# Kernel optimization log

Measured on AMD Instinct MI355X. Metric: run time of the kernel, lower is better.

## Reference

```python
import jax, jax.numpy as jnp
import numpy as np

# SLAYER neuron / simulation constants (from netParams yaml)
THETA = 10.0      # spike threshold
TAU_SR = 10.0     # PSP (SRM) time constant, ms
TS = 1.0          # simulation time step, ms
TAU_RHO = 1.0     # surrogate-gradient width
SCALE_RHO = 1.0   # surrogate-gradient scale
N_TIME_BINS = 300 # tSample / Ts


@jax.custom_vjp
def spike_fn(u):
    # Hard threshold forward; surrogate gradient backward (SLAYER escape-rate pdf).
    return (u >= THETA).astype(u.dtype)

def _spike_fwd(u):
    return spike_fn(u), u

def _spike_bwd(u, g):
    return (g * SCALE_RHO * jnp.exp(-jnp.abs(u - THETA) / TAU_RHO),)

spike_fn.defvjp(_spike_fwd, _spike_bwd)


def psp(x):
    # Causal leaky-integrator (first-order SRM) filter over time.
    # x: [B, T, F] -> u[t] = decay * u[t-1] + x[t]
    decay = jnp.exp(jnp.asarray(-TS / TAU_SR, x.dtype))
    xT = jnp.swapaxes(x, 0, 1)  # [T, B, F]
    def step(u, xt):
        u = decay * u + xt
        return u, u
    _, out = jax.lax.scan(step, jnp.zeros_like(xT[0]), xT)
    return jnp.swapaxes(out, 0, 1)  # [B, T, F]


def rate_encode(inp, n_time_bins, key):
    # Bernoulli rate coding: spike prob per time bin = pixel intensity in [0,1].
    # inp: [B, C, H, W] -> spikes: [B, T, C*H*W]
    B = inp.shape[0]
    probs = inp.reshape(B, 1, -1)  # [B, 1, F]
    u = jax.random.uniform(key, (B, n_time_bins, probs.shape[-1]), dtype=inp.dtype)
    return (u < probs).astype(inp.dtype)


def setup_inputs() -> dict:
    key = jax.random.key(0)
    k1, k2, k3 = jax.random.split(key, 3)
    B, C, H, W = 32, 3, 32, 32
    F_in, F_hid, F_out = C * H * W, 410, 10
    inp = jax.random.uniform(k1, (B, C, H, W), dtype=jnp.float32)
    W1 = jax.random.normal(k2, (F_hid, F_in), dtype=jnp.float32) / np.sqrt(F_in).astype(np.float32)
    W2 = jax.random.normal(k3, (F_out, F_hid), dtype=jnp.float32) / np.sqrt(F_hid).astype(np.float32)
    return {"inp": inp, "W1": W1, "W2": W2}


def reference(inp, W1, W2):
    spikes = rate_encode(inp, N_TIME_BINS, jax.random.key(42))   # [B, T, 3072]
    a1 = jnp.einsum('btf,of->bto', spikes, W1)                    # dense per time bin
    s1 = spike_fn(psp(a1))                                        # [B, T, 410]
    a2 = jnp.einsum('btf,of->bto', s1, W2)
    s2 = spike_fn(psp(a2))                                        # [B, T, 10]
    return jnp.swapaxes(s2, 1, 2)                                 # [B, 10, T]
```

## Files before the change

kernel.cpp:

```cpp
#include <hip/hip_runtime.h>
#include <stdint.h>

#define B_SZ 32
#define T_SZ 300
#define F_IN 3072
#define F_HID 410
#define F_OUT 10
#define M_SZ (B_SZ * T_SZ)
#define N_PAD 448
#define KW (F_IN / 32)
#define TOTAL_ELEMS (B_SZ * T_SZ * F_IN)
#define N_WORDS (TOTAL_ELEMS / 32)
#define A2_STRIDE 16
#define NCHUNK 10
#define CLEN 30
#define NKB (F_IN / 256)
#define MT_CNT (M_SZ / 64)
#define W1_BLOCKS 672
#define RNG_BLOCKS 14400

#define DECAY 0.90483741803595957f
#define THETA 10.0f
#define KS2 (0x1BD11BDAu ^ 42u)

typedef __attribute__((ext_vector_type(8))) int i32x8;
typedef __attribute__((ext_vector_type(16))) float f32x16;

#define TF_R(r) { x0 += x1; \
  asm("v_alignbit_b32 %0, %1, %1, %2" : "=v"(x1) : "v"(x1), "n"(32 - (r))); \
  x1 ^= x0; }

__device__ __forceinline__ uint32_t tf_bits(uint32_t x1i) {
  uint32_t x0 = 0u, x1 = x1i;
  TF_R(13) TF_R(15) TF_R(26) TF_R(6)
  x0 += 42u; x1 += KS2 + 1u;
  TF_R(17) TF_R(29) TF_R(16) TF_R(24)
  x0 += KS2; x1 += 2u;
  TF_R(13) TF_R(15) TF_R(26) TF_R(6)
  x1 += 42u + 3u;
  TF_R(17) TF_R(29) TF_R(16) TF_R(24)
  x0 += 42u; x1 += KS2 + 4u;
  TF_R(13) TF_R(15) TF_R(26) TF_R(6)
  x0 += KS2; x1 += 5u;
  return x0 ^ x1;
}

__device__ __forceinline__ void gld16(const void* g, void* l) {
  __builtin_amdgcn_global_load_lds(
      (const __attribute__((address_space(1))) uint32_t*)g,
      (__attribute__((address_space(3))) uint32_t*)l, 16, 0, 0);
}

__global__ __launch_bounds__(256) void prep(const float* __restrict__ inp,
                                            const float* __restrict__ W1,
                                            uint8_t* __restrict__ W1s,
                                            uint32_t* __restrict__ sbitsT) {
  if (blockIdx.x < W1_BLOCKS) {
    int idx = blockIdx.x * 256 + threadIdx.x;
    int g = idx * 8;
    int n = g / F_IN;
    int k = g - n * F_IN;
    uint32_t d0 = 0u, d1 = 0u;
    if (n < F_HID) {
      const float* s = W1 + (size_t)n * F_IN + k;
      float4 v0 = ((const float4*)s)[0];
      float4 v1 = ((const float4*)s)[1];
      int t0 = __builtin_amdgcn_cvt_pk_fp8_f32(v0.x, v0.y, 0, false);
      t0 = __builtin_amdgcn_cvt_pk_fp8_f32(v0.z, v0.w, t0, true);
      int t1 = __builtin_amdgcn_cvt_pk_fp8_f32(v1.x, v1.y, 0, false);
      t1 = __builtin_amdgcn_cvt_pk_fp8_f32(v1.z, v1.w, t1, true);
      d0 = (uint32_t)t0; d1 = (uint32_t)t1;
    }
    int nt = n >> 6, r = n & 63;
    int kb = k >> 8, c = (k >> 4) & 15, half = (k >> 3) & 1;
    size_t dst = ((((size_t)nt * NKB + kb) * 64 + r) * 16 + (c ^ (r & 15))) * 16 + half * 8;
    *(uint2*)(W1s + dst) = make_uint2(d0, d1);
  } else {
    uint32_t idx = (blockIdx.x - W1_BLOCKS) * 256u + threadIdx.x;
    uint32_t q = idx & 3u;
    uint32_t j = idx >> 2;
    uint32_t r = j & 63u;
    uint32_t t1 = j >> 6;
    uint32_t wi = t1 & 7u;
    uint32_t t2 = t1 >> 3;
    uint32_t kb = t2 % (uint32_t)NKB;
    uint32_t mt = t2 / (uint32_t)NKB;
    uint32_t m = mt * 64u + r;
    uint32_t b = m / (uint32_t)T_SZ;
    uint32_t f = (kb * 8u + wi) * 32u + q * 8u;
    const float* p = inp + b * F_IN + f;
    float4 va = ((const float4*)p)[0];
    float4 vb = ((const float4*)p)[1];
    uint32_t T0 = (uint32_t)ceilf(va.x * 8388608.0f);
    uint32_t T1 = (uint32_t)ceilf(va.y * 8388608.0f);
    uint32_t T2 = (uint32_t)ceilf(va.z * 8388608.0f);
    uint32_t T3 = (uint32_t)ceilf(va.w * 8388608.0f);
    uint32_t T4 = (uint32_t)ceilf(vb.x * 8388608.0f);
    uint32_t T5 = (uint32_t)ceilf(vb.y * 8388608.0f);
    uint32_t T6 = (uint32_t)ceilf(vb.z * 8388608.0f);
    uint32_t T7 = (uint32_t)ceilf(vb.w * 8388608.0f);
    uint32_t b42 = m * (uint32_t)F_IN + f + 42u;
    uint32_t w = 0u;
#define GEN(jj, Tn) { uint32_t bits = tf_bits(b42 + (jj)); \
  w |= ((bits >> 9) < (Tn)) ? (1u << (jj)) : 0u; }
    GEN(0, T0) GEN(1, T1) GEN(2, T2) GEN(3, T3)
    GEN(4, T4) GEN(5, T5) GEN(6, T6) GEN(7, T7)
#undef GEN
    ((uint8_t*)sbitsT)[idx] = (uint8_t)w;
  }
}

__global__ __launch_bounds__(256) void gemm1(const uint32_t* __restrict__ sbitsT,
                                             const uint8_t* __restrict__ W1s,
                                             float* __restrict__ a1) {
  __shared__ uint32_t sAT[8 * 64];
  __shared__ uint8_t sB[64 * 256];

  const int tid = threadIdx.x;
  const int mtile = blockIdx.x;
  const int nt = blockIdx.y;
  const int m0 = mtile * 64;
  const int n0 = nt * 64;
  const int wv = tid >> 6, lane = tid & 63;
  const int wm = (wv & 1) * 32, wn = (wv >> 1) * 32;
  const int l31 = lane & 31, lh = lane >> 5;

  const uint8_t* gB0 = W1s + (size_t)nt * NKB * 16384;
  const uint8_t* gA0 = (const uint8_t*)sbitsT + (size_t)mtile * NKB * 2048;

  f32x16 acc;
#pragma unroll
  for (int e = 0; e < 16; ++e) acc[e] = 0.0f;

  for (int kb = 0; kb < NKB; ++kb) {
    const uint8_t* gB = gB0 + (size_t)kb * 16384;
#pragma unroll
    for (int q = 0; q < 4; ++q)
      gld16(gB + (wv * 4 + q) * 1024 + lane * 16, &sB[(wv * 4 + q) * 1024]);
    if (wv < 2)
      gld16(gA0 + (size_t)kb * 2048 + wv * 1024 + lane * 16,
            (uint8_t*)sAT + wv * 1024);
    __syncthreads();
#pragma unroll
    for (int sub = 0; sub < 4; ++sub) {
      int row = wn + l31;
      int cb = sub * 4 + lh * 2;
      uint4 u0 = *(uint4*)&sB[row * 256 + (((cb + 0) ^ (row & 15)) << 4)];
      uint4 u1 = *(uint4*)&sB[row * 256 + (((cb + 1) ^ (row & 15)) << 4)];
      i32x8 bfr;
      bfr[0] = u0.x; bfr[1] = u0.y; bfr[2] = u0.z; bfr[3] = u0.w;
      bfr[4] = u1.x; bfr[5] = u1.y; bfr[6] = u1.z; bfr[7] = u1.w;
      uint32_t w = sAT[(sub * 2 + lh) * 64 + wm + l31];
      i32x8 afr;
#pragma unroll
      for (int j = 0; j < 8; ++j) {
        uint32_t n = (w >> (4 * j)) & 15u;
        afr[j] = (int)(((n * 0x204081u) & 0x01010101u) * 0x38u);
      }
      acc = __builtin_amdgcn_mfma_scale_f32_32x32x64_f8f6f4(
          afr, bfr, acc, 0, 0, 0, 127, 0, 127);
    }
    __syncthreads();
  }
  int col = n0 + wn + l31;
#pragma unroll
  for (int rg = 0; rg < 16; ++rg) {
    int row = m0 + wm + (rg & 3) + 8 * (rg >> 2) + 4 * lh;
    a1[(size_t)row * N_PAD + col] = acc[rg];
  }
}

__global__ __launch_bounds__(256) void psp1_partial(float* __restrict__ a1,
                                                    float* __restrict__ fin) {
  int idx = blockIdx.x * 256 + threadIdx.x;
  if (idx >= B_SZ * NCHUNK * N_PAD) return;
  int o = idx % N_PAD;
  int bc = idx / N_PAD;
  int c = bc % NCHUNK;
  int b = bc / NCHUNK;
  float* p = a1 + ((size_t)(b * T_SZ + c * CLEN)) * N_PAD + o;
  float u = 0.0f;
#pragma unroll
  for (int i = 0; i < CLEN; ++i) {
    u = __fadd_rn(__fmul_rn(DECAY, u), p[(size_t)i * N_PAD]);
    p[(size_t)i * N_PAD] = u;
  }
  fin[(size_t)bc * N_PAD + o] = u;
}

__global__ __launch_bounds__(256) void apply_gemm2(const float* __restrict__ a1,
                                                   const float* __restrict__ fin,
                                                   const float* __restrict__ W2,
                                                   float* __restrict__ a2) {
  __shared__ float sW2[F_OUT * F_HID];
  for (int i = threadIdx.x; i < F_OUT * F_HID; i += 256) sW2[i] = W2[i];
  __syncthreads();
  int m = blockIdx.x * 4 + (threadIdx.x >> 6);
  int lane = threadIdx.x & 63;
  int b = m / T_SZ, t = m % T_SZ;
  int c = t / CLEN, tl = t % CLEN;
  float d30 = 1.0f;
#pragma unroll
  for (int i = 0; i < CLEN; ++i) d30 *= DECAY;
  float dp = DECAY;
  for (int i = 0; i < tl; ++i) dp *= DECAY;
  float p[F_OUT];
#pragma unroll
  for (int o = 0; o < F_OUT; ++o) p[o] = 0.0f;
#pragma unroll
  for (int j = 0; j < 7; ++j) {
    int hh = lane + j * 64;
    float u = a1[(size_t)m * N_PAD + hh];
    if (c > 0) {
      float F = 0.0f;
      const float* f = fin + (size_t)b * NCHUNK * N_PAD + hh;
      for (int cc = 0; cc < c; ++cc)
        F = f[(size_t)cc * N_PAD] + d30 * F;
      u = __fadd_rn(u, __fmul_rn(dp, F));
    }
    bool valid = hh < F_HID;
    float s = (u >= THETA && valid) ? 1.0f : 0.0f;
    int hcl = valid ? hh : 0;
#pragma unroll
    for (int o = 0; o < F_OUT; ++o) p[o] = fmaf(s, sW2[o * F_HID + hcl], p[o]);
  }
#pragma unroll
  for (int o = 0; o < F_OUT; ++o)
#pragma unroll
    for (int s = 1; s < 64; s <<= 1) p[o] += __shfl_xor(p[o], s, 64);
  if (lane < F_OUT) a2[(size_t)m * A2_STRIDE + lane] = p[lane];
}

__global__ __launch_bounds__(128) void psp2(const float* __restrict__ a2,
                                            float* __restrict__ out) {
  __shared__ float chf[NCHUNK][F_OUT];
  __shared__ float seed[NCHUNK][F_OUT];
  int b = blockIdx.x;
  int tid = threadIdx.x;
  int o = tid / NCHUNK, c = tid % NCHUNK;
  const float* p = a2 + ((size_t)(b * T_SZ + c * CLEN)) * A2_STRIDE + o;
  float v[CLEN];
  float pa[CLEN];
  if (tid < F_OUT * NCHUNK) {
#pragma unroll
    for (int i = 0; i < CLEN; ++i) v[i] = p[(size_t)i * A2_STRIDE];
    float u = 0.0f;
#pragma unroll
    for (int i = 0; i < CLEN; ++i) {
      u = __fadd_rn(__fmul_rn(DECAY, u), v[i]);
      pa[i] = u;
    }
    chf[c][o] = u;
  }
  __syncthreads();
  if (tid < F_OUT) {
    float d30 = 1.0f;
#pragma unroll
    for (int i = 0; i < CLEN; ++i) d30 *= DECAY;
    float F = 0.0f;
    for (int cc = 0; cc < NCHUNK; ++cc) {
      F = chf[cc][tid] + d30 * F;
      seed[cc][tid] = F;
    }
  }
  __syncthreads();
  if (tid < F_OUT * NCHUNK) {
    float F = (c == 0) ? 0.0f : seed[c - 1][o];
    float dp = DECAY;
    float* q = out + (size_t)b * F_OUT * T_SZ + (size_t)o * T_SZ + c * CLEN;
#pragma unroll
    for (int i = 0; i < CLEN; ++i) {
      float u = (c == 0) ? pa[i] : __fadd_rn(pa[i], __fmul_rn(dp, F));
      q[i] = (u >= THETA) ? 1.0f : 0.0f;
      dp *= DECAY;
    }
  }
}

extern "C" void kernel_launch(void* const* d_in, const int* in_sizes, int n_in,
                              void* d_out, int out_size, void* d_ws, size_t ws_size,
                              hipStream_t stream) {
  const float* inp = (const float*)d_in[0];
  const float* W1  = (const float*)d_in[1];
  const float* W2  = (const float*)d_in[2];
  float* out = (float*)d_out;
  char* ws = (char*)d_ws;
  uint8_t* W1s = (uint8_t*)(ws);
  uint32_t* sbitsT = (uint32_t*)(ws + 1376256);
  float* a1 = (float*)(ws + 1376256 + 3686400);
  float* fin = a1 + (size_t)M_SZ * N_PAD;
  float* a2 = fin + (size_t)B_SZ * NCHUNK * N_PAD;

  prep<<<dim3(W1_BLOCKS + RNG_BLOCKS), dim3(256), 0, stream>>>(inp, W1, W1s, sbitsT);
  gemm1<<<dim3(MT_CNT, N_PAD / 64), dim3(256), 0, stream>>>(sbitsT, W1s, a1);
  psp1_partial<<<dim3((B_SZ * NCHUNK * N_PAD) / 256), dim3(256), 0, stream>>>(a1, fin);
  apply_gemm2<<<dim3(M_SZ / 4), dim3(256), 0, stream>>>(a1, fin, W2, a2);
  psp2<<<dim3(B_SZ), dim3(128), 0, stream>>>(a2, out);
}
```

Measured before the change: 173.5 us.

## Fuse gemm1, psp1, gemm2 and psp2 into one persistent kernel with grid barriers

```diff
diff --git a/kernel.cpp b/kernel.cpp
--- a/kernel.cpp
+++ b/kernel.cpp
@@ -16,6 +16,7 @@
 #define CLEN 30
 #define NKB (F_IN / 256)
 #define MT_CNT (M_SZ / 64)
+#define NTILES (MT_CNT * (N_PAD / 64))
 #define W1_BLOCKS 672
 #define RNG_BLOCKS 14400
 
@@ -54,7 +55,9 @@
 __global__ __launch_bounds__(256) void prep(const float* __restrict__ inp,
                                             const float* __restrict__ W1,
                                             uint8_t* __restrict__ W1s,
-                                            uint32_t* __restrict__ sbitsT) {
+                                            uint32_t* __restrict__ sbitsT,
+                                            unsigned long long* __restrict__ bar) {
+  if (blockIdx.x == 0 && threadIdx.x < 3) bar[threadIdx.x] = 0ull;
   if (blockIdx.x < W1_BLOCKS) {
     int idx = blockIdx.x * 256 + threadIdx.x;
     int g = idx * 8;
@@ -110,169 +113,189 @@
   }
 }
 
-__global__ __launch_bounds__(256) void gemm1(const uint32_t* __restrict__ sbitsT,
-                                             const uint8_t* __restrict__ W1s,
-                                             float* __restrict__ a1) {
-  __shared__ uint32_t sAT[8 * 64];
-  __shared__ uint8_t sB[64 * 256];
-
+__device__ __forceinline__ void gbar(unsigned long long* c) {
+  __syncthreads();
+  if (threadIdx.x == 0) {
+    __threadfence();
+    unsigned long long t = atomicAdd(c, 1ull);
+    unsigned long long g = (unsigned long long)gridDim.x;
+    unsigned long long tgt = t - (t % g) + g;
+    while (atomicAdd(c, 0ull) < tgt) __builtin_amdgcn_s_sleep(4);
+  }
+  __syncthreads();
+  __threadfence();
+}
+
+__global__ __launch_bounds__(256, 2) void mega(
+    const uint32_t* __restrict__ sbitsT, const uint8_t* __restrict__ W1s,
+    float* __restrict__ a1, float* __restrict__ fin,
+    const float* __restrict__ W2, float* __restrict__ a2,
+    float* __restrict__ out, unsigned long long* __restrict__ bar) {
+  __shared__ __align__(16) char smem[18432];
   const int tid = threadIdx.x;
-  const int mtile = blockIdx.x;
-  const int nt = blockIdx.y;
-  const int m0 = mtile * 64;
-  const int n0 = nt * 64;
-  const int wv = tid >> 6, lane = tid & 63;
-  const int wm = (wv & 1) * 32, wn = (wv >> 1) * 32;
-  const int l31 = lane & 31, lh = lane >> 5;
-
-  const uint8_t* gB0 = W1s + (size_t)nt * NKB * 16384;
-  const uint8_t* gA0 = (const uint8_t*)sbitsT + (size_t)mtile * NKB * 2048;
-
-  f32x16 acc;
-#pragma unroll
-  for (int e = 0; e < 16; ++e) acc[e] = 0.0f;
-
-  for (int kb = 0; kb < NKB; ++kb) {
-    const uint8_t* gB = gB0 + (size_t)kb * 16384;
-#pragma unroll
-    for (int q = 0; q < 4; ++q)
-      gld16(gB + (wv * 4 + q) * 1024 + lane * 16, &sB[(wv * 4 + q) * 1024]);
-    if (wv < 2)
-      gld16(gA0 + (size_t)kb * 2048 + wv * 1024 + lane * 16,
-            (uint8_t*)sAT + wv * 1024);
+  const int NB = gridDim.x;
+
+  {
+    uint32_t* sAT = (uint32_t*)smem;
+    uint8_t* sB = (uint8_t*)(smem + 2048);
+    const int wv = tid >> 6, lane = tid & 63;
+    const int wm = (wv & 1) * 32, wn = (wv >> 1) * 32;
+    const int l31 = lane & 31, lh = lane >> 5;
+    for (int vb = blockIdx.x; vb < NTILES; vb += NB) {
+      const int mtile = vb % MT_CNT;
+      const int nt = vb / MT_CNT;
+      const int m0 = mtile * 64;
+      const int n0 = nt * 64;
+      const uint8_t* gB0 = W1s + (size_t)nt * NKB * 16384;
+      const uint8_t* gA0 = (const uint8_t*)sbitsT + (size_t)mtile * NKB * 2048;
+
+      f32x16 acc;
+#pragma unroll
+      for (int e = 0; e < 16; ++e) acc[e] = 0.0f;
+
+      for (int kb = 0; kb < NKB; ++kb) {
+        const uint8_t* gB = gB0 + (size_t)kb * 16384;
+#pragma unroll
+        for (int q = 0; q < 4; ++q)
+          gld16(gB + (wv * 4 + q) * 1024 + lane * 16, &sB[(wv * 4 + q) * 1024]);
+        if (wv < 2)
+          gld16(gA0 + (size_t)kb * 2048 + wv * 1024 + lane * 16,
+                (uint8_t*)sAT + wv * 1024);
+        __syncthreads();
+#pragma unroll
+        for (int sub = 0; sub < 4; ++sub) {
+          int row = wn + l31;
+          int cb = sub * 4 + lh * 2;
+          uint4 u0 = *(uint4*)&sB[row * 256 + (((cb + 0) ^ (row & 15)) << 4)];
+          uint4 u1 = *(uint4*)&sB[row * 256 + (((cb + 1) ^ (row & 15)) << 4)];
+          i32x8 bfr;
+          bfr[0] = u0.x; bfr[1] = u0.y; bfr[2] = u0.z; bfr[3] = u0.w;
+          bfr[4] = u1.x; bfr[5] = u1.y; bfr[6] = u1.z; bfr[7] = u1.w;
+          uint32_t w = sAT[(sub * 2 + lh) * 64 + wm + l31];
+          i32x8 afr;
+#pragma unroll
+          for (int j = 0; j < 8; ++j) {
+            uint32_t n = (w >> (4 * j)) & 15u;
+            afr[j] = (int)(((n * 0x204081u) & 0x01010101u) * 0x38u);
+          }
+          acc = __builtin_amdgcn_mfma_scale_f32_32x32x64_f8f6f4(
+              afr, bfr, acc, 0, 0, 0, 127, 0, 127);
+        }
+        __syncthreads();
+      }
+      int col = n0 + wn + l31;
+#pragma unroll
+      for (int rg = 0; rg < 16; ++rg) {
+        int row = m0 + wm + (rg & 3) + 8 * (rg >> 2) + 4 * lh;
+        a1[(size_t)row * N_PAD + col] = acc[rg];
+      }
+    }
+  }
+  gbar(bar + 0);
+
+  for (int idx = blockIdx.x * 256 + tid; idx < B_SZ * NCHUNK * N_PAD;
+       idx += NB * 256) {
+    int o = idx % N_PAD;
+    int bc = idx / N_PAD;
+    int c = bc % NCHUNK;
+    int b = bc / NCHUNK;
+    float* p = a1 + ((size_t)(b * T_SZ + c * CLEN)) * N_PAD + o;
+    float u = 0.0f;
+#pragma unroll
+    for (int i = 0; i < CLEN; ++i) {
+      u = __fadd_rn(__fmul_rn(DECAY, u), p[(size_t)i * N_PAD]);
+      p[(size_t)i * N_PAD] = u;
+    }
+    fin[(size_t)bc * N_PAD + o] = u;
+  }
+  gbar(bar + 1);
+
+  {
+    float* sW2 = (float*)smem;
+    for (int i = tid; i < F_OUT * F_HID; i += 256) sW2[i] = W2[i];
     __syncthreads();
-#pragma unroll
-    for (int sub = 0; sub < 4; ++sub) {
-      int row = wn + l31;
-      int cb = sub * 4 + lh * 2;
-      uint4 u0 = *(uint4*)&sB[row * 256 + (((cb + 0) ^ (row & 15)) << 4)];
-      uint4 u1 = *(uint4*)&sB[row * 256 + (((cb + 1) ^ (row & 15)) << 4)];
-      i32x8 bfr;
-      bfr[0] = u0.x; bfr[1] = u0.y; bfr[2] = u0.z; bfr[3] = u0.w;
-      bfr[4] = u1.x; bfr[5] = u1.y; bfr[6] = u1.z; bfr[7] = u1.w;
-      uint32_t w = sAT[(sub * 2 + lh) * 64 + wm + l31];
-      i32x8 afr;
-#pragma unroll
-      for (int j = 0; j < 8; ++j) {
-        uint32_t n = (w >> (4 * j)) & 15u;
-        afr[j] = (int)(((n * 0x204081u) & 0x01010101u) * 0x38u);
-      }
-      acc = __builtin_amdgcn_mfma_scale_f32_32x32x64_f8f6f4(
-          afr, bfr, acc, 0, 0, 0, 127, 0, 127);
-    }
-    __syncthreads();
-  }
-  int col = n0 + wn + l31;
-#pragma unroll
-  for (int rg = 0; rg < 16; ++rg) {
-    int row = m0 + wm + (rg & 3) + 8 * (rg >> 2) + 4 * lh;
-    a1[(size_t)row * N_PAD + col] = acc[rg];
-  }
-}
-
-__global__ __launch_bounds__(256) void psp1_partial(float* __restrict__ a1,
-                                                    float* __restrict__ fin) {
-  int idx = blockIdx.x * 256 + threadIdx.x;
-  if (idx >= B_SZ * NCHUNK * N_PAD) return;
-  int o = idx % N_PAD;
-  int bc = idx / N_PAD;
-  int c = bc % NCHUNK;
-  int b = bc / NCHUNK;
-  float* p = a1 + ((size_t)(b * T_SZ + c * CLEN)) * N_PAD + o;
-  float u = 0.0f;
-#pragma unroll
-  for (int i = 0; i < CLEN; ++i) {
-    u = __fadd_rn(__fmul_rn(DECAY, u), p[(size_t)i * N_PAD]);
-    p[(size_t)i * N_PAD] = u;
-  }
-  fin[(size_t)bc * N_PAD + o] = u;
-}
-
-__global__ __launch_bounds__(256) void apply_gemm2(const float* __restrict__ a1,
-                                                   const float* __restrict__ fin,
-                                                   const float* __restrict__ W2,
-                                                   float* __restrict__ a2) {
-  __shared__ float sW2[F_OUT * F_HID];
-  for (int i = threadIdx.x; i < F_OUT * F_HID; i += 256) sW2[i] = W2[i];
-  __syncthreads();
-  int m = blockIdx.x * 4 + (threadIdx.x >> 6);
-  int lane = threadIdx.x & 63;
-  int b = m / T_SZ, t = m % T_SZ;
-  int c = t / CLEN, tl = t % CLEN;
-  float d30 = 1.0f;
-#pragma unroll
-  for (int i = 0; i < CLEN; ++i) d30 *= DECAY;
-  float dp = DECAY;
-  for (int i = 0; i < tl; ++i) dp *= DECAY;
-  float p[F_OUT];
-#pragma unroll
-  for (int o = 0; o < F_OUT; ++o) p[o] = 0.0f;
-#pragma unroll
-  for (int j = 0; j < 7; ++j) {
-    int hh = lane + j * 64;
-    float u = a1[(size_t)m * N_PAD + hh];
-    if (c > 0) {
-      float F = 0.0f;
-      const float* f = fin + (size_t)b * NCHUNK * N_PAD + hh;
-      for (int cc = 0; cc < c; ++cc)
-        F = f[(size_t)cc * N_PAD] + d30 * F;
-      u = __fadd_rn(u, __fmul_rn(dp, F));
-    }
-    bool valid = hh < F_HID;
-    float s = (u >= THETA && valid) ? 1.0f : 0.0f;
-    int hcl = valid ? hh : 0;
-#pragma unroll
-    for (int o = 0; o < F_OUT; ++o) p[o] = fmaf(s, sW2[o * F_HID + hcl], p[o]);
-  }
-#pragma unroll
-  for (int o = 0; o < F_OUT; ++o)
-#pragma unroll
-    for (int s = 1; s < 64; s <<= 1) p[o] += __shfl_xor(p[o], s, 64);
-  if (lane < F_OUT) a2[(size_t)m * A2_STRIDE + lane] = p[lane];
-}
-
-__global__ __launch_bounds__(128) void psp2(const float* __restrict__ a2,
-                                            float* __restrict__ out) {
-  __shared__ float chf[NCHUNK][F_OUT];
-  __shared__ float seed[NCHUNK][F_OUT];
-  int b = blockIdx.x;
-  int tid = threadIdx.x;
-  int o = tid / NCHUNK, c = tid % NCHUNK;
-  const float* p = a2 + ((size_t)(b * T_SZ + c * CLEN)) * A2_STRIDE + o;
-  float v[CLEN];
-  float pa[CLEN];
-  if (tid < F_OUT * NCHUNK) {
-#pragma unroll
-    for (int i = 0; i < CLEN; ++i) v[i] = p[(size_t)i * A2_STRIDE];
-    float u = 0.0f;
-#pragma unroll
-    for (int i = 0; i < CLEN; ++i) {
-      u = __fadd_rn(__fmul_rn(DECAY, u), v[i]);
-      pa[i] = u;
-    }
-    chf[c][o] = u;
-  }
-  __syncthreads();
-  if (tid < F_OUT) {
+    const int lane = tid & 63;
     float d30 = 1.0f;
 #pragma unroll
     for (int i = 0; i < CLEN; ++i) d30 *= DECAY;
-    float F = 0.0f;
-    for (int cc = 0; cc < NCHUNK; ++cc) {
-      F = chf[cc][tid] + d30 * F;
-      seed[cc][tid] = F;
-    }
-  }
-  __syncthreads();
-  if (tid < F_OUT * NCHUNK) {
-    float F = (c == 0) ? 0.0f : seed[c - 1][o];
-    float dp = DECAY;
-    float* q = out + (size_t)b * F_OUT * T_SZ + (size_t)o * T_SZ + c * CLEN;
-#pragma unroll
-    for (int i = 0; i < CLEN; ++i) {
-      float u = (c == 0) ? pa[i] : __fadd_rn(pa[i], __fmul_rn(dp, F));
-      q[i] = (u >= THETA) ? 1.0f : 0.0f;
-      dp *= DECAY;
+    for (int vb = blockIdx.x; vb < M_SZ / 4; vb += NB) {
+      int m = vb * 4 + (tid >> 6);
+      int b = m / T_SZ, t = m % T_SZ;
+      int ch = t / CLEN, tl = t % CLEN;
+      float dp = DECAY;
+      for (int i = 0; i < tl; ++i) dp *= DECAY;
+      float p[F_OUT];
+#pragma unroll
+      for (int o = 0; o < F_OUT; ++o) p[o] = 0.0f;
+#pragma unroll
+      for (int j = 0; j < 7; ++j) {
+        int hh = lane + j * 64;
+        float u = a1[(size_t)m * N_PAD + hh];
+        if (ch > 0) {
+          float F = 0.0f;
+          const float* f = fin + (size_t)b * NCHUNK * N_PAD + hh;
+          for (int cc = 0; cc < ch; ++cc)
+            F = f[(size_t)cc * N_PAD] + d30 * F;
+          u = __fadd_rn(u, __fmul_rn(dp, F));
+        }
+        bool valid = hh < F_HID;
+        float s = (u >= THETA && valid) ? 1.0f : 0.0f;
+        int hcl = valid ? hh : 0;
+#pragma unroll
+        for (int o = 0; o < F_OUT; ++o) p[o] = fmaf(s, sW2[o * F_HID + hcl], p[o]);
+      }
+#pragma unroll
+      for (int o = 0; o < F_OUT; ++o)
+#pragma unroll
+        for (int s = 1; s < 64; s <<= 1) p[o] += __shfl_xor(p[o], s, 64);
+      if (lane < F_OUT) a2[(size_t)m * A2_STRIDE + lane] = p[lane];
+    }
+  }
+  gbar(bar + 2);
+
+  {
+    float (*chf)[F_OUT] = (float (*)[F_OUT])smem;
+    float (*seed)[F_OUT] = (float (*)[F_OUT])(smem + sizeof(float) * NCHUNK * F_OUT);
+    for (int vb = blockIdx.x; vb < B_SZ; vb += NB) {
+      int b = vb;
+      int o = tid / NCHUNK, cc = tid % NCHUNK;
+      const float* p = a2 + ((size_t)(b * T_SZ + cc * CLEN)) * A2_STRIDE + o;
+      float v[CLEN];
+      float pa[CLEN];
+      if (tid < F_OUT * NCHUNK) {
+#pragma unroll
+        for (int i = 0; i < CLEN; ++i) v[i] = p[(size_t)i * A2_STRIDE];
+        float u = 0.0f;
+#pragma unroll
+        for (int i = 0; i < CLEN; ++i) {
+          u = __fadd_rn(__fmul_rn(DECAY, u), v[i]);
+          pa[i] = u;
+        }
+        chf[cc][o] = u;
+      }
+      __syncthreads();
+      if (tid < F_OUT) {
+        float d30 = 1.0f;
+#pragma unroll
+        for (int i = 0; i < CLEN; ++i) d30 *= DECAY;
+        float F = 0.0f;
+        for (int c2 = 0; c2 < NCHUNK; ++c2) {
+          F = chf[c2][tid] + d30 * F;
+          seed[c2][tid] = F;
+        }
+      }
+      __syncthreads();
+      if (tid < F_OUT * NCHUNK) {
+        float F = (cc == 0) ? 0.0f : seed[cc - 1][o];
+        float dp = DECAY;
+        float* q = out + (size_t)b * F_OUT * T_SZ + (size_t)o * T_SZ + cc * CLEN;
+#pragma unroll
+        for (int i = 0; i < CLEN; ++i) {
+          float u = (cc == 0) ? pa[i] : __fadd_rn(pa[i], __fmul_rn(dp, F));
+          q[i] = (u >= THETA) ? 1.0f : 0.0f;
+          dp *= DECAY;
+        }
+      }
     }
   }
 }
@@ -290,10 +313,17 @@
   float* a1 = (float*)(ws + 1376256 + 3686400);
   float* fin = a1 + (size_t)M_SZ * N_PAD;
   float* a2 = fin + (size_t)B_SZ * NCHUNK * N_PAD;
-
-  prep<<<dim3(W1_BLOCKS + RNG_BLOCKS), dim3(256), 0, stream>>>(inp, W1, W1s, sbitsT);
-  gemm1<<<dim3(MT_CNT, N_PAD / 64), dim3(256), 0, stream>>>(sbitsT, W1s, a1);
-  psp1_partial<<<dim3((B_SZ * NCHUNK * N_PAD) / 256), dim3(256), 0, stream>>>(a1, fin);
-  apply_gemm2<<<dim3(M_SZ / 4), dim3(256), 0, stream>>>(a1, fin, W2, a2);
-  psp2<<<dim3(B_SZ), dim3(128), 0, stream>>>(a2, out);
-}
+  unsigned long long* bar = (unsigned long long*)((char*)a2 + 40);
+
+  static int NBLK = 0;
+  if (NBLK == 0) {
+    int t = 0;
+    if (hipOccupancyMaxActiveBlocksPerMultiprocessor(&t, mega, 256, 0) != hipSuccess)
+      t = 2;
+    if (t < 2) t = 2;
+    NBLK = (t >= 3) ? 525 : 350;
+  }
+
+  prep<<<dim3(W1_BLOCKS + RNG_BLOCKS), dim3(256), 0, stream>>>(inp, W1, W1s, sbitsT, bar);
+  mega<<<dim3(NBLK), dim3(256), 0, stream>>>(sbitsT, W1s, a1, fin, W2, a2, out, bar);
+}
```

Result: slower. 386.3 us (+122.7%).
